# Performance work log

Hardware: AMD Instinct MI355X
Metric: run time of the kernel (lower is better)

## Reference

```python
import jax, jax.numpy as jnp
import numpy as np

B, N, EB, NA, DIM, NIT = 256, 128, 5, 64, 512, 3  # EB = n_bonds + 1 (channel 0 = no-bond, dropped)


def setup_inputs() -> dict:
    key = jax.random.key(0)
    ks = jax.random.split(key, 10)
    adj = jax.random.uniform(ks[0], (B, N, N, EB), dtype=jnp.float32)
    node = jax.random.normal(ks[1], (B, N, NA), dtype=jnp.float32)
    hidden = jnp.zeros((B, N, DIM), dtype=jnp.float32)  # accepted but unused by forward
    # nn.Linear default init: U(-1/sqrt(fan_in), 1/sqrt(fan_in))
    se = 1.0 / np.sqrt(NA)
    sd = 1.0 / np.sqrt(DIM)
    W_embed = jax.random.uniform(ks[2], (NA, DIM), minval=-se, maxval=se, dtype=jnp.float32)
    b_embed = jax.random.uniform(ks[3], (DIM,), minval=-se, maxval=se, dtype=jnp.float32)
    W_layers = jax.random.uniform(ks[4], (NIT, DIM, DIM), minval=-sd, maxval=sd, dtype=jnp.float32)
    b_layers = jax.random.uniform(ks[5], (NIT, DIM), minval=-sd, maxval=sd, dtype=jnp.float32)
    W_out = jax.random.uniform(ks[6], (DIM, 1), minval=-sd, maxval=sd, dtype=jnp.float32)
    b_out = jax.random.uniform(ks[7], (1,), minval=-sd, maxval=sd, dtype=jnp.float32)
    return {"adj": adj, "hidden": hidden, "node": node,
            "W_embed": W_embed, "b_embed": b_embed,
            "W_layers": W_layers, "b_layers": b_layers,
            "W_out": W_out, "b_out": b_out}


def reference(adj, hidden, node, W_embed, b_embed, W_layers, b_layers, W_out, b_out):
    # adj[:, :, :, 1:].permute(0, 3, 1, 2) -> [B, E, N, N]
    a = jnp.transpose(adj[..., 1:], (0, 3, 1, 2))
    h = node @ W_embed + b_embed  # [B, N, DIM]
    for i in range(NIT):  # WLSLinearLayer: relu(Linear(h + sum_e adj_e @ h))
        agg = jnp.einsum('benm,bmd->bnd', a, h)  # sum over bond types of neighbor aggregation
        h = jax.nn.relu((h + agg) @ W_layers[i] + b_layers[i])
    graph_repr = jnp.mean(h, axis=1)  # [B, DIM]
    logit = graph_repr @ W_out + b_out  # [B, 1], activation=None path
    return (logit, graph_repr)
```

## Files before the change

### kernel.cpp

```cpp
#include <hip/hip_runtime.h>
#include <hip/hip_bf16.h>


typedef __bf16 bf16;
typedef __bf16 bf16x4 __attribute__((ext_vector_type(4)));
typedef __bf16 bf16x8 __attribute__((ext_vector_type(8)));
typedef float floatx4 __attribute__((ext_vector_type(4)));


__global__ __launch_bounds__(256) void k_pack(const float* __restrict__ We,
                                              const float* __restrict__ Wl,
                                              bf16* __restrict__ PWe,
                                              bf16* __restrict__ PWl) {
    __shared__ float S[512][17];
    int z = blockIdx.y, td = blockIdx.x;
    const float* src; bf16* dst; int K;
    if (z < 3) { src = Wl + (size_t)z * 262144; dst = PWl + (size_t)z * 262144; K = 512; }
    else       { src = We;                      dst = PWe;                      K = 64; }
    int tid = threadIdx.x;
    int x = tid & 15, y = tid >> 4;
    for (int kb = 0; kb < K; kb += 16) {
        int k = kb + y;
        S[k][x] = src[(size_t)k * 512 + td * 16 + x];
    }
    __syncthreads();
    int lane = tid & 63, w = tid >> 6, q = lane >> 4, l16 = lane & 15;
    int KT = K >> 5;
    for (int tk = w; tk < KT; tk += 4) {
        bf16x8 v;
#pragma unroll
        for (int j = 0; j < 8; j++) v[j] = (bf16)S[tk * 32 + q * 8 + j][l16];
        *(bf16x8*)&dst[(size_t)((td * KT + tk) * 64 + lane) * 8] = v;
    }
}

__global__ __launch_bounds__(1024, 4) void k_mega(
    const float* __restrict__ adj,
    const float* __restrict__ nodef,
    const bf16* __restrict__ PWe,
    const float* __restrict__ b_embed,
    const bf16* __restrict__ PWl,
    const float* __restrict__ b_layers,
    const float* __restrict__ W_out,
    const float* __restrict__ b_out,
    float* __restrict__ out)
{
    __shared__ __align__(16) char pool[163840];
    bf16* HT = (bf16*)pool;
    bf16* AhatP = (bf16*)(pool + 131072);

    const int b = blockIdx.x;
    const int tid = threadIdx.x;
    const int lane = tid & 63, wid = tid >> 6;
    const int q = lane >> 4, l16 = lane & 15;

    {
        const float4* srcb = (const float4*)(adj + (size_t)b * 81920);
#pragma unroll
        for (int p = 0; p < 4; p++) {
            int t = p * 1024 + tid;
            const float4* ptr = srcb + (size_t)t * 5;
            float4 v0 = ptr[0], v1 = ptr[1], v2 = ptr[2], v3 = ptr[3], v4 = ptr[4];
            float s0 = v0.y + v0.z + v0.w + v1.x;
            float s1 = v1.z + v1.w + v2.x + v2.y;
            float s2 = v2.w + v3.x + v3.y + v3.z;
            float s3 = v4.x + v4.y + v4.z + v4.w;
            int n = t >> 5, m0 = (t & 31) * 4;
            bf16x4 o;
            o[0] = (bf16)(s0 + ((n == m0 + 0) ? 1.f : 0.f));
            o[1] = (bf16)(s1 + ((n == m0 + 1) ? 1.f : 0.f));
            o[2] = (bf16)(s2 + ((n == m0 + 2) ? 1.f : 0.f));
            o[3] = (bf16)(s3 + ((n == m0 + 3) ? 1.f : 0.f));
            int ntG = n >> 4, l16n = n & 15;
            int kk = m0 >> 5, mq = (m0 & 31) >> 3, half = (m0 >> 2) & 1;
            int cphys = mq * 16 + (l16n ^ (mq * 2));
            *(bf16x4*)&AhatP[(size_t)(((ntG * 4 + kk) * 64 + cphys) * 8 + half * 4)] = o;
        }
    }

    {
        const int wmE = wid >> 3, wnE = wid & 7;
        const float* Ab = nodef + (size_t)b * 8192;
        floatx4 accE[4][4] = {};
#pragma unroll
        for (int kk = 0; kk < 2; kk++) {
            bf16x8 af[4], bfr[4];
#pragma unroll
            for (int mt = 0; mt < 4; mt++) {
                const float* srcp = Ab + (size_t)(wmE * 64 + mt * 16 + l16) * 64 + kk * 32 + q * 8;
                float4 x = *(const float4*)srcp;
                float4 y = *(const float4*)(srcp + 4);
                bf16x8 v;
                v[0] = (bf16)x.x; v[1] = (bf16)x.y; v[2] = (bf16)x.z; v[3] = (bf16)x.w;
                v[4] = (bf16)y.x; v[5] = (bf16)y.y; v[6] = (bf16)y.z; v[7] = (bf16)y.w;
                af[mt] = v;
            }
#pragma unroll
            for (int nt = 0; nt < 4; nt++) {
                int td = wnE * 4 + nt;
                bfr[nt] = *(const bf16x8*)&PWe[(size_t)((td * 2 + kk) * 64 + lane) * 8];
            }
            __builtin_amdgcn_s_setprio(1);
#pragma unroll
            for (int mt = 0; mt < 4; mt++)
#pragma unroll
                for (int nt = 0; nt < 4; nt++)
                    accE[mt][nt] = __builtin_amdgcn_mfma_f32_16x16x32_bf16(af[mt], bfr[nt], accE[mt][nt], 0, 0, 0);
            __builtin_amdgcn_s_setprio(0);
        }
#pragma unroll
        for (int mt = 0; mt < 4; mt++)
#pragma unroll
            for (int nt = 0; nt < 4; nt++) {
                int d = wnE * 64 + nt * 16 + l16;
                float bv = b_embed[d];
                int c = wmE * 8 + mt * 2 + (q >> 1);
                int off = ((c ^ (d & 15)) << 3) + (q & 1) * 4;
                bf16x4 pk;
#pragma unroll
                for (int r = 0; r < 4; r++) pk[r] = (bf16)(accE[mt][nt][r] + bv);
                *(bf16x4*)&HT[d * 128 + off] = pk;
            }
    }
    __syncthreads();

    const int nh = wid & 1, dg = wid >> 1;
    const int pc = lane ^ ((lane >> 4) * 2);

    for (int it = 0; it < 3; it++) {
        const bf16* WT = PWl + (size_t)it * 262144;
        const float* bl = b_layers + it * 512;

        const bf16* Wb0 = WT + (size_t)(wid * 2 + 0) * 8192 + lane * 8;
        const bf16* Wb1 = WT + (size_t)(wid * 2 + 1) * 8192 + lane * 8;

        bf16x8 w00 = *(const bf16x8*)Wb0;
        bf16x8 w01 = *(const bf16x8*)Wb1;

        floatx4 at[4][4] = {};
#pragma unroll
        for (int kk = 0; kk < 4; kk++) {
            bf16x8 bfr[4];
#pragma unroll
            for (int nt = 0; nt < 4; nt++)
                bfr[nt] = *(const bf16x8*)&AhatP[(size_t)(((nh * 4 + nt) * 4 + kk) * 64 + pc) * 8];
            bf16x8 afr[4];
#pragma unroll
            for (int dt = 0; dt < 4; dt++) {
                int drow = dg * 64 + dt * 16 + l16;
                int off = ((4 * kk + q) ^ (drow & 15)) << 3;
                afr[dt] = *(const bf16x8*)&HT[drow * 128 + off];
            }
            __builtin_amdgcn_s_setprio(1);
#pragma unroll
            for (int dt = 0; dt < 4; dt++)
#pragma unroll
                for (int nt = 0; nt < 4; nt++)
                    at[dt][nt] = __builtin_amdgcn_mfma_f32_16x16x32_bf16(afr[dt], bfr[nt], at[dt][nt], 0, 0, 0);
            __builtin_amdgcn_s_setprio(0);
        }
        __syncthreads();
        {
#pragma unroll
            for (int dt = 0; dt < 4; dt++)
#pragma unroll
                for (int nt = 0; nt < 4; nt++) {
                    int n = nh * 64 + nt * 16 + l16;
                    int c = dg * 8 + dt * 2 + (q >> 1);
                    int off = ((c ^ l16) << 3) + (q & 1) * 4;
                    bf16x4 pk;
#pragma unroll
                    for (int r = 0; r < 4; r++) pk[r] = (bf16)at[dt][nt][r];
                    *(bf16x4*)&HT[n * 512 + off] = pk;
                }
        }
        __syncthreads();

        floatx4 acc[8][2] = {};
        bf16x8 w10 = *(const bf16x8*)(Wb0 + 512);
        bf16x8 w11 = *(const bf16x8*)(Wb1 + 512);
        for (int dc = 0; dc < 16; dc++) {
            int dcn = (dc + 2) & 15;
            bf16x8 n0 = *(const bf16x8*)(Wb0 + dcn * 512);
            bf16x8 n1 = *(const bf16x8*)(Wb1 + dcn * 512);
            int c = ((dc * 4 + q) ^ l16) << 3;
            bf16x8 afa[4];
#pragma unroll
            for (int mt = 0; mt < 4; mt++)
                afa[mt] = *(const bf16x8*)&HT[(mt * 16 + l16) * 512 + c];
            __builtin_amdgcn_s_setprio(1);
#pragma unroll
            for (int mt = 0; mt < 4; mt++)
                acc[mt][0] = __builtin_amdgcn_mfma_f32_16x16x32_bf16(afa[mt], w00, acc[mt][0], 0, 0, 0);
#pragma unroll
            for (int mt = 0; mt < 4; mt++)
                acc[mt][1] = __builtin_amdgcn_mfma_f32_16x16x32_bf16(afa[mt], w01, acc[mt][1], 0, 0, 0);
            __builtin_amdgcn_s_setprio(0);
            bf16x8 afb[4];
#pragma unroll
            for (int mt = 0; mt < 4; mt++)
                afb[mt] = *(const bf16x8*)&HT[((mt + 4) * 16 + l16) * 512 + c];
            __builtin_amdgcn_s_setprio(1);
#pragma unroll
            for (int mt = 0; mt < 4; mt++)
                acc[mt + 4][0] = __builtin_amdgcn_mfma_f32_16x16x32_bf16(afb[mt], w00, acc[mt + 4][0], 0, 0, 0);
#pragma unroll
            for (int mt = 0; mt < 4; mt++)
                acc[mt + 4][1] = __builtin_amdgcn_mfma_f32_16x16x32_bf16(afb[mt], w01, acc[mt + 4][1], 0, 0, 0);
            __builtin_amdgcn_s_setprio(0);
            w00 = w10; w01 = w11; w10 = n0; w11 = n1;
        }

        if (it < 2) {
            __syncthreads();
#pragma unroll
            for (int nt = 0; nt < 2; nt++) {
                int dp = wid * 32 + nt * 16 + l16;
                float bv = bl[dp];
#pragma unroll
                for (int mt = 0; mt < 8; mt++) {
                    int c = mt * 2 + (q >> 1);
                    int off = ((c ^ (dp & 15)) << 3) + (q & 1) * 4;
                    bf16x4 pk;
#pragma unroll
                    for (int r = 0; r < 4; r++) pk[r] = (bf16)fmaxf(acc[mt][nt][r] + bv, 0.f);
                    *(bf16x4*)&HT[dp * 128 + off] = pk;
                }
            }
            __syncthreads();
        } else {
            float* RsF = (float*)(pool + 131072);
#pragma unroll
            for (int nt = 0; nt < 2; nt++) {
                int dp = wid * 32 + nt * 16 + l16;
                float bv = bl[dp];
                float s = 0.f;
#pragma unroll
                for (int mt = 0; mt < 8; mt++)
#pragma unroll
                    for (int r = 0; r < 4; r++)
                        s += fmaxf(acc[mt][nt][r] + bv, 0.f);
                s += __shfl_down(s, 32);
                s += __shfl_down(s, 16);
                if (lane < 16) RsF[dp] = s;
            }
        }
    }
    __syncthreads();

    float* RsF = (float*)(pool + 131072);
    float* lpF = (float*)(pool + 131072 + 2048);
    if (tid < 512) {
        float g = RsF[tid] * (1.f / 128.f);
        out[256 + (size_t)b * 512 + tid] = g;
        lpF[tid] = g * W_out[tid];
    }
    __syncthreads();
    if (wid == 0) {
        float s = 0.f;
#pragma unroll
        for (int k = 0; k < 8; k++) s += lpF[lane + k * 64];
        s += __shfl_down(s, 32);
        s += __shfl_down(s, 16);
        s += __shfl_down(s, 8);
        s += __shfl_down(s, 4);
        s += __shfl_down(s, 2);
        s += __shfl_down(s, 1);
        if (lane == 0) out[b] = s + b_out[0];
    }
}

extern "C" void kernel_launch(void* const* d_in, const int* in_sizes, int n_in,
                              void* d_out, int out_size, void* d_ws, size_t ws_size,
                              hipStream_t stream) {
    const float* adj      = (const float*)d_in[0];
    const float* node     = (const float*)d_in[2];
    const float* W_embed  = (const float*)d_in[3];
    const float* b_embed  = (const float*)d_in[4];
    const float* W_layers = (const float*)d_in[5];
    const float* b_layers = (const float*)d_in[6];
    const float* W_out    = (const float*)d_in[7];
    const float* b_out    = (const float*)d_in[8];
    float* out = (float*)d_out;

    char* ws = (char*)d_ws;
    bf16* PWe = (bf16*)(ws);
    bf16* PWl = (bf16*)(ws + 65536);

    k_pack<<<dim3(32, 4), 256, 0, stream>>>(W_embed, W_layers, PWe, PWl);
    k_mega<<<256, 1024, 0, stream>>>(adj, node, PWe, b_embed, PWl, b_layers,
                                     W_out, b_out, out);
}
```

Baseline: 240.8 us.

## Align warp tiling with output columns so aggregation writes need fewer barriers

```diff
diff --git a/kernel.cpp b/kernel.cpp
--- a/kernel.cpp
+++ b/kernel.cpp
@@ -79,52 +79,51 @@
     }
 
     {
-        const int wmE = wid >> 3, wnE = wid & 7;
         const float* Ab = nodef + (size_t)b * 8192;
-        floatx4 accE[4][4] = {};
+        floatx4 accE[8][2] = {};
 #pragma unroll
         for (int kk = 0; kk < 2; kk++) {
-            bf16x8 af[4], bfr[4];
-#pragma unroll
-            for (int mt = 0; mt < 4; mt++) {
-                const float* srcp = Ab + (size_t)(wmE * 64 + mt * 16 + l16) * 64 + kk * 32 + q * 8;
-                float4 x = *(const float4*)srcp;
-                float4 y = *(const float4*)(srcp + 4);
-                bf16x8 v;
-                v[0] = (bf16)x.x; v[1] = (bf16)x.y; v[2] = (bf16)x.z; v[3] = (bf16)x.w;
-                v[4] = (bf16)y.x; v[5] = (bf16)y.y; v[6] = (bf16)y.z; v[7] = (bf16)y.w;
-                af[mt] = v;
-            }
-#pragma unroll
-            for (int nt = 0; nt < 4; nt++) {
-                int td = wnE * 4 + nt;
-                bfr[nt] = *(const bf16x8*)&PWe[(size_t)((td * 2 + kk) * 64 + lane) * 8];
-            }
-            __builtin_amdgcn_s_setprio(1);
-#pragma unroll
-            for (int mt = 0; mt < 4; mt++)
-#pragma unroll
-                for (int nt = 0; nt < 4; nt++)
-                    accE[mt][nt] = __builtin_amdgcn_mfma_f32_16x16x32_bf16(af[mt], bfr[nt], accE[mt][nt], 0, 0, 0);
-            __builtin_amdgcn_s_setprio(0);
-        }
-#pragma unroll
-        for (int mt = 0; mt < 4; mt++)
-#pragma unroll
-            for (int nt = 0; nt < 4; nt++) {
-                int d = wnE * 64 + nt * 16 + l16;
-                float bv = b_embed[d];
-                int c = wmE * 8 + mt * 2 + (q >> 1);
+            bf16x8 bfr[2];
+#pragma unroll
+            for (int nt = 0; nt < 2; nt++)
+                bfr[nt] = *(const bf16x8*)&PWe[(size_t)(((wid * 2 + nt) * 2 + kk) * 64 + lane) * 8];
+#pragma unroll
+            for (int half = 0; half < 2; half++) {
+                bf16x8 af[4];
+#pragma unroll
+                for (int mt = 0; mt < 4; mt++) {
+                    const float* srcp = Ab + (size_t)((half * 4 + mt) * 16 + l16) * 64 + kk * 32 + q * 8;
+                    float4 x = *(const float4*)srcp;
+                    float4 y = *(const float4*)(srcp + 4);
+                    bf16x8 v;
+                    v[0] = (bf16)x.x; v[1] = (bf16)x.y; v[2] = (bf16)x.z; v[3] = (bf16)x.w;
+                    v[4] = (bf16)y.x; v[5] = (bf16)y.y; v[6] = (bf16)y.z; v[7] = (bf16)y.w;
+                    af[mt] = v;
+                }
+#pragma unroll
+                for (int mt = 0; mt < 4; mt++)
+#pragma unroll
+                    for (int nt = 0; nt < 2; nt++)
+                        accE[half * 4 + mt][nt] = __builtin_amdgcn_mfma_f32_16x16x32_bf16(af[mt], bfr[nt], accE[half * 4 + mt][nt], 0, 0, 0);
+            }
+        }
+#pragma unroll
+        for (int nt = 0; nt < 2; nt++) {
+            int d = wid * 32 + nt * 16 + l16;
+            float bv = b_embed[d];
+#pragma unroll
+            for (int mt = 0; mt < 8; mt++) {
+                int c = mt * 2 + (q >> 1);
                 int off = ((c ^ (d & 15)) << 3) + (q & 1) * 4;
                 bf16x4 pk;
 #pragma unroll
                 for (int r = 0; r < 4; r++) pk[r] = (bf16)(accE[mt][nt][r] + bv);
                 *(bf16x4*)&HT[d * 128 + off] = pk;
             }
-    }
-    __syncthreads();
-
-    const int nh = wid & 1, dg = wid >> 1;
+        }
+    }
+    __syncthreads();
+
     const int pc = lane ^ ((lane >> 4) * 2);
 
     for (int it = 0; it < 3; it++) {
@@ -136,58 +135,59 @@
 
         bf16x8 w00 = *(const bf16x8*)Wb0;
         bf16x8 w01 = *(const bf16x8*)Wb1;
-
-        floatx4 at[4][4] = {};
+        bf16x8 w10 = *(const bf16x8*)(Wb0 + 512);
+        bf16x8 w11 = *(const bf16x8*)(Wb1 + 512);
+
+        floatx4 at[2][8] = {};
 #pragma unroll
         for (int kk = 0; kk < 4; kk++) {
-            bf16x8 bfr[4];
-#pragma unroll
-            for (int nt = 0; nt < 4; nt++)
-                bfr[nt] = *(const bf16x8*)&AhatP[(size_t)(((nh * 4 + nt) * 4 + kk) * 64 + pc) * 8];
-            bf16x8 afr[4];
-#pragma unroll
-            for (int dt = 0; dt < 4; dt++) {
-                int drow = dg * 64 + dt * 16 + l16;
+            bf16x8 afr[2];
+#pragma unroll
+            for (int dt = 0; dt < 2; dt++) {
+                int drow = wid * 32 + dt * 16 + l16;
                 int off = ((4 * kk + q) ^ (drow & 15)) << 3;
                 afr[dt] = *(const bf16x8*)&HT[drow * 128 + off];
             }
-            __builtin_amdgcn_s_setprio(1);
-#pragma unroll
-            for (int dt = 0; dt < 4; dt++)
+#pragma unroll
+            for (int g = 0; g < 2; g++) {
+                bf16x8 bfr[4];
 #pragma unroll
                 for (int nt = 0; nt < 4; nt++)
-                    at[dt][nt] = __builtin_amdgcn_mfma_f32_16x16x32_bf16(afr[dt], bfr[nt], at[dt][nt], 0, 0, 0);
-            __builtin_amdgcn_s_setprio(0);
+                    bfr[nt] = *(const bf16x8*)&AhatP[(size_t)(((g * 4 + nt) * 4 + kk) * 64 + pc) * 8];
+                __builtin_amdgcn_s_setprio(1);
+#pragma unroll
+                for (int nt = 0; nt < 4; nt++)
+#pragma unroll
+                    for (int dt = 0; dt < 2; dt++)
+                        at[dt][g * 4 + nt] = __builtin_amdgcn_mfma_f32_16x16x32_bf16(afr[dt], bfr[nt], at[dt][g * 4 + nt], 0, 0, 0);
+                __builtin_amdgcn_s_setprio(0);
+            }
+        }
+        {
+            bf16* Treg = HT + wid * 4096;
+#pragma unroll
+            for (int dt = 0; dt < 2; dt++)
+#pragma unroll
+                for (int nt = 0; nt < 8; nt++) {
+                    int n = nt * 16 + l16;
+                    bf16x4 pk;
+#pragma unroll
+                    for (int r = 0; r < 4; r++) pk[r] = (bf16)at[dt][nt][r];
+                    *(bf16x4*)&Treg[(dt * 2 + (q >> 1)) * 1024 + n * 8 + (q & 1) * 4] = pk;
+                }
         }
         __syncthreads();
-        {
-#pragma unroll
-            for (int dt = 0; dt < 4; dt++)
-#pragma unroll
-                for (int nt = 0; nt < 4; nt++) {
-                    int n = nh * 64 + nt * 16 + l16;
-                    int c = dg * 8 + dt * 2 + (q >> 1);
-                    int off = ((c ^ l16) << 3) + (q & 1) * 4;
-                    bf16x4 pk;
-#pragma unroll
-                    for (int r = 0; r < 4; r++) pk[r] = (bf16)at[dt][nt][r];
-                    *(bf16x4*)&HT[n * 512 + off] = pk;
-                }
-        }
-        __syncthreads();
 
         floatx4 acc[8][2] = {};
-        bf16x8 w10 = *(const bf16x8*)(Wb0 + 512);
-        bf16x8 w11 = *(const bf16x8*)(Wb1 + 512);
         for (int dc = 0; dc < 16; dc++) {
             int dcn = (dc + 2) & 15;
             bf16x8 n0 = *(const bf16x8*)(Wb0 + dcn * 512);
             bf16x8 n1 = *(const bf16x8*)(Wb1 + dcn * 512);
-            int c = ((dc * 4 + q) ^ l16) << 3;
+            const bf16* Tdc = HT + dc * 4096 + q * 1024 + l16 * 8;
             bf16x8 afa[4];
 #pragma unroll
             for (int mt = 0; mt < 4; mt++)
-                afa[mt] = *(const bf16x8*)&HT[(mt * 16 + l16) * 512 + c];
+                afa[mt] = *(const bf16x8*)&Tdc[mt * 128];
             __builtin_amdgcn_s_setprio(1);
 #pragma unroll
             for (int mt = 0; mt < 4; mt++)
@@ -199,7 +199,7 @@
             bf16x8 afb[4];
 #pragma unroll
             for (int mt = 0; mt < 4; mt++)
-                afb[mt] = *(const bf16x8*)&HT[((mt + 4) * 16 + l16) * 512 + c];
+                afb[mt] = *(const bf16x8*)&Tdc[(mt + 4) * 128];
             __builtin_amdgcn_s_setprio(1);
 #pragma unroll
             for (int mt = 0; mt < 4; mt++)
@@ -227,7 +227,6 @@
                     *(bf16x4*)&HT[dp * 128 + off] = pk;
                 }
             }
-            __syncthreads();
         } else {
             float* RsF = (float*)(pool + 131072);
 #pragma unroll
```

After: 231.6 us. -3.8%, faster.
